# Optimization experiments

Hardware: AMD Instinct MI355X
Metric: run time of the kernel (lower is better)

The kernel has to match this reference:

```python
import jax, jax.numpy as jnp
import numpy as np

H = 200  # LSTM units per layer
SEQ_LEN = 100
NUM_AXIS = 4


def setup_inputs() -> dict:
    key = jax.random.key(0)
    ks = jax.random.split(key, 12)
    B = 8192
    s = 0.05  # small init scale to avoid gate saturation
    inp = {
        "x": jax.random.normal(ks[0], (B, SEQ_LEN, 1), dtype=jnp.float32),
        # layer 0: input dim 1
        "W0": jax.random.normal(ks[1], (1, 4 * H), dtype=jnp.float32) * s,
        "U0": jax.random.normal(ks[2], (H, 4 * H), dtype=jnp.float32) * s,
        "b0": jax.random.normal(ks[3], (4 * H,), dtype=jnp.float32) * s,
        # layer 1
        "W1": jax.random.normal(ks[4], (H, 4 * H), dtype=jnp.float32) * s,
        "U1": jax.random.normal(ks[5], (H, 4 * H), dtype=jnp.float32) * s,
        "b1": jax.random.normal(ks[6], (4 * H,), dtype=jnp.float32) * s,
        # layer 2
        "W2": jax.random.normal(ks[7], (H, 4 * H), dtype=jnp.float32) * s,
        "U2": jax.random.normal(ks[8], (H, 4 * H), dtype=jnp.float32) * s,
        "b2": jax.random.normal(ks[9], (4 * H,), dtype=jnp.float32) * s,
        # dense head: 200 -> 400, tanh
        "Wfc": jax.random.normal(ks[10], (H, SEQ_LEN * NUM_AXIS), dtype=jnp.float32) * s,
        "bfc": jax.random.normal(ks[11], (SEQ_LEN * NUM_AXIS,), dtype=jnp.float32) * s,
    }
    return inp


def _lstm_step(h, c, xt, W, U, b):
    # Keras LSTMCell gate order: i, f, g(candidate), o
    z = xt @ W + h @ U + b  # [B, 4H]
    i, f, g, o = jnp.split(z, 4, axis=-1)
    c_new = jax.nn.sigmoid(f) * c + jax.nn.sigmoid(i) * jnp.tanh(g)
    h_new = jax.nn.sigmoid(o) * jnp.tanh(c_new)
    return h_new, c_new


def reference(x, W0, U0, b0, W1, U1, b1, W2, U2, b2, Wfc, bfc):
    B = x.shape[0]
    zeros = jnp.zeros((B, H), dtype=x.dtype)
    carry0 = (zeros, zeros, zeros, zeros, zeros, zeros)

    def step(carry, xt):
        h0, c0, h1, c1, h2, c2 = carry
        h0, c0 = _lstm_step(h0, c0, xt, W0, U0, b0)
        h1, c1 = _lstm_step(h1, c1, h0, W1, U1, b1)
        h2, c2 = _lstm_step(h2, c2, h1, W2, U2, b2)
        return (h0, c0, h1, c1, h2, c2), None

    # scan over time: x is [B, T, 1] -> [T, B, 1]
    xs = jnp.swapaxes(x, 0, 1)
    (h0, c0, h1, c1, h2, c2), _ = jax.lax.scan(step, carry0, xs)
    # return_sequences=False -> final top-layer hidden state
    y = jnp.tanh(h2 @ Wfc + bfc)  # [B, 400]
    return y.reshape(B, SEQ_LEN, NUM_AXIS)
```

## Files before the change

kernel.cpp:

```cpp
#include <hip/hip_runtime.h>

#define Hdim 200
#define NP   800
#define Tlen 100
#define BT   32
#define KB   7
#define HS   232
#define NT   50
#define THREADS 768
#define CHSTR (NT*64*8)
#define MATSZ (KB*CHSTR)

#define WAIT_LGKM0 0xC07F

typedef float f32x4 __attribute__((ext_vector_type(4)));
typedef short s16x8 __attribute__((ext_vector_type(8)));

__device__ __forceinline__ ushort f2bf(float f) {
    unsigned u = __float_as_uint(f);
    return (ushort)((u + 0x7fffu + ((u >> 16) & 1u)) >> 16);
}
__device__ __forceinline__ float bf2f(ushort s) {
    return __uint_as_float(((unsigned)s) << 16);
}
__device__ __forceinline__ float sigmoid_fast(float v) {
    return 1.0f / (1.0f + __expf(-v));
}
__device__ __forceinline__ float tanh_fast(float v) {
    return 2.0f / (1.0f + __expf(-2.0f * v)) - 1.0f;
}
__device__ __forceinline__ void wg_barrier() {
    asm volatile("" ::: "memory");
    __builtin_amdgcn_s_waitcnt(WAIT_LGKM0);
    __builtin_amdgcn_s_barrier();
    asm volatile("" ::: "memory");
}

__global__ void pack_weights(const float* __restrict__ U0, const float* __restrict__ W1,
                             const float* __restrict__ U1, const float* __restrict__ W2,
                             const float* __restrict__ U2, ushort* __restrict__ dst) {
    int idx = blockIdx.x * blockDim.x + threadIdx.x;
    if (idx >= 5 * KB * NT * 64) return;
    int lane = idx & 63; int rest = idx >> 6;
    int nt = rest % NT; rest /= NT;
    int kb = rest % KB; int mi = rest / KB;
    const float* src = (mi == 0) ? U0 : (mi == 1) ? W1 : (mi == 2) ? U1 : (mi == 3) ? W2 : U2;
    int np = nt * 16 + (lane & 15);
    int ncol = (np & 3) * Hdim + (np >> 2);
    int k0 = kb * 32 + (lane >> 4) * 8;
    ushort v[8];
#pragma unroll
    for (int j = 0; j < 8; ++j) {
        int k = k0 + j;
        v[j] = (k < Hdim) ? f2bf(src[k * NP + ncol]) : (ushort)0;
    }
    uint4 o;
    o.x = (unsigned)v[0] | ((unsigned)v[1] << 16);
    o.y = (unsigned)v[2] | ((unsigned)v[3] << 16);
    o.z = (unsigned)v[4] | ((unsigned)v[5] << 16);
    o.w = (unsigned)v[6] | ((unsigned)v[7] << 16);
    ((uint4*)dst)[idx] = o;
}

template<int CHW>
__device__ __forceinline__ void stage_chunk(const ushort* gp, ushort* dstbuf, int lane) {
#pragma unroll
    for (int mt = 0; mt < CHW; ++mt) {
        __builtin_amdgcn_global_load_lds(
            (const __attribute__((address_space(1))) void*)(gp + (size_t)mt * 512 + lane * 8),
            (__attribute__((address_space(3))) void*)(dstbuf + mt * 512),
            16, 0, 0);
    }
}

__device__ __forceinline__ void unpack4(const ushort* p, float (&o)[4]) {
    uint2 u = *(const uint2*)p;
    o[0] = bf2f((ushort)(u.x));  o[1] = bf2f((ushort)(u.x >> 16));
    o[2] = bf2f((ushort)(u.y));  o[3] = bf2f((ushort)(u.y >> 16));
}

template<int CHW>
__device__ __forceinline__ void gate_phase(f32x4 (&acc)[2][CHW],
                                           float (&creg)[2][CHW],
                                           ushort* __restrict__ hbl,
                                           int lane, int S_w) {
    const int l15 = lane & 15, q = lane >> 4;
#pragma unroll
    for (int nt = 0; nt < 2; ++nt) {
#pragma unroll
        for (int mt = 0; mt < CHW; ++mt) {
            const int u = (S_w + mt) * 4 + q;
            const int n = nt * 16 + l15;
            f32x4 z = acc[nt][mt];
            float iv = sigmoid_fast(z[0]);
            float fv = sigmoid_fast(z[1]);
            float gv = tanh_fast(z[2]);
            float ov = sigmoid_fast(z[3]);
            float c = fv * creg[nt][mt] + iv * gv;
            creg[nt][mt] = c;
            hbl[n * HS + u] = f2bf(ov * tanh_fast(c));
        }
    }
}

template<int CHW>
__device__ __forceinline__ void run_slots(int s0, int s1, int t,
        ushort* __restrict__ sl, f32x4 (&acc)[2][CHW],
        const ushort* __restrict__ pk, const uint* gTab, const uint* bhTab,
        const ushort* hbflat, int bhbase, int lane, int& isl) {
#pragma unroll 1
    for (int s = s0; s < s1; ++s) {
        __builtin_amdgcn_s_waitcnt(0x0F70 | CHW);
        ushort* buf = sl + ((t + s) & 1) * (CHW * 512);
        s16x8 frag[CHW];
#pragma unroll
        for (int mt = 0; mt < CHW; ++mt)
            frag[mt] = *(const s16x8*)(buf + mt * 512 + lane * 8);
        const ushort* bp = hbflat + bhTab[s] + bhbase;
        s16x8 bh0 = *(const s16x8*)bp;
        s16x8 bh1 = *(const s16x8*)(bp + 16 * HS);
#pragma unroll
        for (int mt = 0; mt < CHW; ++mt) {
            acc[0][mt] = __builtin_amdgcn_mfma_f32_16x16x32_bf16(frag[mt], bh0, acc[0][mt], 0, 0, 0);
            acc[1][mt] = __builtin_amdgcn_mfma_f32_16x16x32_bf16(frag[mt], bh1, acc[1][mt], 0, 0, 0);
        }
        __builtin_amdgcn_s_waitcnt(WAIT_LGKM0);
        stage_chunk<CHW>(pk + gTab[isl], buf, lane);
        isl = (isl == 34) ? 0 : isl + 1;
    }
}

template<int CHW>
__device__ __forceinline__ void time_loop(const int S_w, const int lane,
        const int bhbase, ushort* __restrict__ sl, const ushort* __restrict__ pk,
        const uint* gTab, const uint* bhTab, ushort* __restrict__ hbflat,
        const ushort (&pbwb)[4][NP], const ushort (&xTs)[Tlen][BT]) {
    const int l15 = lane & 15, q = lane >> 4;

    float creg[3][2][CHW];
#pragma unroll
    for (int l = 0; l < 3; ++l)
#pragma unroll
        for (int nt = 0; nt < 2; ++nt)
#pragma unroll
            for (int mt = 0; mt < CHW; ++mt) creg[l][nt][mt] = 0.0f;

    stage_chunk<CHW>(pk + gTab[0], sl, lane);
    stage_chunk<CHW>(pk + gTab[1], sl + CHW * 512, lane);
    int isl = 2;

    for (int t = 0; t < Tlen; ++t) {
        f32x4 acc[2][CHW];

        const float xn0 = bf2f(xTs[t][l15]);
        const float xn1 = bf2f(xTs[t][16 + l15]);
#pragma unroll
        for (int mt = 0; mt < CHW; ++mt) {
            const int row = (S_w + mt) * 16 + q * 4;
            float bb[4], ww[4];
            unpack4(&pbwb[0][row], bb);
            unpack4(&pbwb[3][row], ww);
#pragma unroll
            for (int r = 0; r < 4; ++r) {
                acc[0][mt][r] = fmaf(xn0, ww[r], bb[r]);
                acc[1][mt][r] = fmaf(xn1, ww[r], bb[r]);
            }
        }

        run_slots<CHW>(0, 7, t, sl, acc, pk, gTab, bhTab, hbflat, bhbase, lane, isl);
        wg_barrier();
        gate_phase<CHW>(acc, creg[0], hbflat + 0 * BT * HS, lane, S_w);
        wg_barrier();

#pragma unroll
        for (int mt = 0; mt < CHW; ++mt) {
            const int row = (S_w + mt) * 16 + q * 4;
            float bb[4];
            unpack4(&pbwb[1][row], bb);
#pragma unroll
            for (int r = 0; r < 4; ++r) { acc[0][mt][r] = bb[r]; acc[1][mt][r] = bb[r]; }
        }
        run_slots<CHW>(7, 21, t, sl, acc, pk, gTab, bhTab, hbflat, bhbase, lane, isl);
        wg_barrier();
        gate_phase<CHW>(acc, creg[1], hbflat + 1 * BT * HS, lane, S_w);
        wg_barrier();

#pragma unroll
        for (int mt = 0; mt < CHW; ++mt) {
            const int row = (S_w + mt) * 16 + q * 4;
            float bb[4];
            unpack4(&pbwb[2][row], bb);
#pragma unroll
            for (int r = 0; r < 4; ++r) { acc[0][mt][r] = bb[r]; acc[1][mt][r] = bb[r]; }
        }
        run_slots<CHW>(21, 35, t, sl, acc, pk, gTab, bhTab, hbflat, bhbase, lane, isl);
        wg_barrier();
        gate_phase<CHW>(acc, creg[2], hbflat + 2 * BT * HS, lane, S_w);
        wg_barrier();
    }
}

__global__ void __launch_bounds__(THREADS)
lstm3_mfma(const float* __restrict__ x,
           const float* __restrict__ W0, const float* __restrict__ b0,
           const float* __restrict__ b1, const float* __restrict__ b2,
           const float* __restrict__ Wfc, const float* __restrict__ bfc,
           const ushort* __restrict__ packed,
           float* __restrict__ out) {
    __shared__ ushort hb[3][BT][HS];
    __shared__ ushort stage[NT * 1024];
    __shared__ ushort pbwb[4][NP];
    __shared__ ushort xTs[Tlen][BT];
    __shared__ uint   gTab[35];
    __shared__ uint   bhTab[35];

    const int tid = threadIdx.x;
    const int wave = tid >> 6, lane = tid & 63;
    const int bx = blockIdx.x;
    const int bbase = bx * BT;

    for (int i = tid; i < 3 * BT * HS; i += THREADS) ((ushort*)hb)[i] = 0;
    for (int i = tid; i < NP; i += THREADS) {
        int nc = (i & 3) * Hdim + (i >> 2);
        pbwb[0][i] = f2bf(b0[nc]); pbwb[1][i] = f2bf(b1[nc]);
        pbwb[2][i] = f2bf(b2[nc]); pbwb[3][i] = f2bf(W0[nc]);
    }
    for (int i = tid; i < BT * Tlen; i += THREADS) {
        int m = i / Tlen, tt = i % Tlen;
        xTs[tt][m] = f2bf(x[(size_t)(bbase + m) * Tlen + tt]);
    }
    if (tid < 35) {
        int s = tid; uint goff, bhoff;
        if (s < 7) {
            int c = (s + bx) % 7;
            goff = 0u * MATSZ + c * CHSTR;           bhoff = 0u * BT * HS + c * 32;
        } else if (s < 21) {
            int c = (s - 7 + bx) % 14;
            if (c < 7) { goff = 2u * MATSZ + c * CHSTR;       bhoff = 1u * BT * HS + c * 32; }
            else       { goff = 1u * MATSZ + (c - 7) * CHSTR; bhoff = 0u * BT * HS + (c - 7) * 32; }
        } else {
            int c = (s - 21 + bx * 5) % 14;
            if (c < 7) { goff = 4u * MATSZ + c * CHSTR;       bhoff = 2u * BT * HS + c * 32; }
            else       { goff = 3u * MATSZ + (c - 7) * CHSTR; bhoff = 1u * BT * HS + (c - 7) * 32; }
        }
        gTab[s] = goff; bhTab[s] = bhoff;
    }
    __syncthreads();

    const int S_w = (wave < 2) ? wave * 5 : 10 + (wave - 2) * 4;
    const ushort* pk = packed + (size_t)S_w * 512;
    ushort* sl = &stage[S_w * 1024];
    ushort* hbflat = &hb[0][0][0];
    const int bhbase = (lane & 15) * HS + (lane >> 4) * 8;

    if (wave < 2) time_loop<5>(S_w, lane, bhbase, sl, pk, gTab, bhTab, hbflat, pbwb, xTs);
    else          time_loop<4>(S_w, lane, bhbase, sl, pk, gTab, bhTab, hbflat, pbwb, xTs);

    __syncthreads();

    for (int gidx = tid; gidx < BT * 100; gidx += THREADS) {
        int m = gidx / 100;
        int j4 = (gidx % 100) * 4;
        const ushort* h2 = &hb[2][m][0];
        float4 a4 = *(const float4*)(bfc + j4);
        float s0 = a4.x, s1 = a4.y, s2 = a4.z, s3 = a4.w;
        for (int k = 0; k < Hdim; ++k) {
            float hk = bf2f(h2[k]);
            float4 w4 = *(const float4*)(Wfc + (size_t)k * 400 + j4);
            s0 = fmaf(hk, w4.x, s0);
            s1 = fmaf(hk, w4.y, s1);
            s2 = fmaf(hk, w4.z, s2);
            s3 = fmaf(hk, w4.w, s3);
        }
        float4 o4;
        o4.x = tanh_fast(s0); o4.y = tanh_fast(s1);
        o4.z = tanh_fast(s2); o4.w = tanh_fast(s3);
        *(float4*)(out + (size_t)(bbase + m) * 400 + j4) = o4;
    }
}

extern "C" void kernel_launch(void* const* d_in, const int* in_sizes, int n_in,
                              void* d_out, int out_size, void* d_ws, size_t ws_size,
                              hipStream_t stream) {
    const float* x   = (const float*)d_in[0];
    const float* W0  = (const float*)d_in[1];
    const float* U0  = (const float*)d_in[2];
    const float* b0  = (const float*)d_in[3];
    const float* W1  = (const float*)d_in[4];
    const float* U1  = (const float*)d_in[5];
    const float* b1  = (const float*)d_in[6];
    const float* W2  = (const float*)d_in[7];
    const float* U2  = (const float*)d_in[8];
    const float* b2  = (const float*)d_in[9];
    const float* Wfc = (const float*)d_in[10];
    const float* bfc = (const float*)d_in[11];
    float* out = (float*)d_out;
    ushort* packed = (ushort*)d_ws;

    const int B = in_sizes[0] / Tlen;
    const int pack_threads = 5 * KB * NT * 64;
    pack_weights<<<(pack_threads + 255) / 256, 256, 0, stream>>>(U0, W1, U1, W2, U2, packed);
    lstm3_mfma<<<B / BT, THREADS, 0, stream>>>(x, W0, b0, b1, b2, Wfc, bfc, packed, out);
}
```

Before: 2.644 ms.

## Keep two layer-0 weight chunks register-resident and stage Wfc through LDS for head

Each wave now loads its first two layer-0 recurrent weight chunks into registers once and computes those slots without DMA staging. This shrinks the per-step streamed ring from 35 to 33 slots and cuts global weight traffic and staging waits. The dense head is restructured to copy Wfc in 50-row chunks into the freed shared stage buffer, so the batch rows reuse it instead of each thread streaming Wfc from global memory. The cost is higher register pressure from the resident fragments, which could lower occupancy or cause spills.

```diff
diff --git a/kernel.cpp b/kernel.cpp
--- a/kernel.cpp
+++ b/kernel.cpp
@@ -10,6 +10,7 @@
 #define THREADS 768
 #define CHSTR (NT*64*8)
 #define MATSZ (KB*CHSTR)
+#define NRING 33
 
 #define WAIT_LGKM0 0xC07F
 
@@ -103,15 +104,28 @@
     }
 }
 
+template<int CHW, int C>
+__device__ __forceinline__ void res_slot(const s16x8 (&rw)[CHW], f32x4 (&acc)[2][CHW],
+        const ushort* hbflat, int bhbase) {
+    const ushort* bp = hbflat + C * 32 + bhbase;
+    s16x8 bh0 = *(const s16x8*)bp;
+    s16x8 bh1 = *(const s16x8*)(bp + 16 * HS);
+#pragma unroll
+    for (int mt = 0; mt < CHW; ++mt) {
+        acc[0][mt] = __builtin_amdgcn_mfma_f32_16x16x32_bf16(rw[mt], bh0, acc[0][mt], 0, 0, 0);
+        acc[1][mt] = __builtin_amdgcn_mfma_f32_16x16x32_bf16(rw[mt], bh1, acc[1][mt], 0, 0, 0);
+    }
+}
+
 template<int CHW>
-__device__ __forceinline__ void run_slots(int s0, int s1, int t,
+__device__ __forceinline__ void run_dma(int s0, int s1,
         ushort* __restrict__ sl, f32x4 (&acc)[2][CHW],
         const ushort* __restrict__ pk, const uint* gTab, const uint* bhTab,
-        const ushort* hbflat, int bhbase, int lane, int& isl) {
+        const ushort* hbflat, int bhbase, int lane, int& isl, int& par) {
 #pragma unroll 1
     for (int s = s0; s < s1; ++s) {
         __builtin_amdgcn_s_waitcnt(0x0F70 | CHW);
-        ushort* buf = sl + ((t + s) & 1) * (CHW * 512);
+        ushort* buf = sl + par * (CHW * 512);
         s16x8 frag[CHW];
 #pragma unroll
         for (int mt = 0; mt < CHW; ++mt)
@@ -126,7 +140,8 @@
         }
         __builtin_amdgcn_s_waitcnt(WAIT_LGKM0);
         stage_chunk<CHW>(pk + gTab[isl], buf, lane);
-        isl = (isl == 34) ? 0 : isl + 1;
+        isl = (isl == NRING - 1) ? 0 : isl + 1;
+        par ^= 1;
     }
 }
 
@@ -145,9 +160,16 @@
 #pragma unroll
             for (int mt = 0; mt < CHW; ++mt) creg[l][nt][mt] = 0.0f;
 
+    s16x8 rw0[CHW], rw1[CHW];
+#pragma unroll
+    for (int mt = 0; mt < CHW; ++mt) {
+        rw0[mt] = *(const s16x8*)(pk + 0 * CHSTR + mt * 512 + lane * 8);
+        rw1[mt] = *(const s16x8*)(pk + 1 * CHSTR + mt * 512 + lane * 8);
+    }
+
     stage_chunk<CHW>(pk + gTab[0], sl, lane);
     stage_chunk<CHW>(pk + gTab[1], sl + CHW * 512, lane);
-    int isl = 2;
+    int isl = 2, par = 0;
 
     for (int t = 0; t < Tlen; ++t) {
         f32x4 acc[2][CHW];
@@ -167,7 +189,11 @@
             }
         }
 
-        run_slots<CHW>(0, 7, t, sl, acc, pk, gTab, bhTab, hbflat, bhbase, lane, isl);
+        run_dma<CHW>(0, 1, sl, acc, pk, gTab, bhTab, hbflat, bhbase, lane, isl, par);
+        res_slot<CHW, 0>(rw0, acc, hbflat, bhbase);
+        run_dma<CHW>(1, 2, sl, acc, pk, gTab, bhTab, hbflat, bhbase, lane, isl, par);
+        res_slot<CHW, 1>(rw1, acc, hbflat, bhbase);
+        run_dma<CHW>(2, 5, sl, acc, pk, gTab, bhTab, hbflat, bhbase, lane, isl, par);
         wg_barrier();
         gate_phase<CHW>(acc, creg[0], hbflat + 0 * BT * HS, lane, S_w);
         wg_barrier();
@@ -180,7 +206,7 @@
 #pragma unroll
             for (int r = 0; r < 4; ++r) { acc[0][mt][r] = bb[r]; acc[1][mt][r] = bb[r]; }
         }
-        run_slots<CHW>(7, 21, t, sl, acc, pk, gTab, bhTab, hbflat, bhbase, lane, isl);
+        run_dma<CHW>(5, 19, sl, acc, pk, gTab, bhTab, hbflat, bhbase, lane, isl, par);
         wg_barrier();
         gate_phase<CHW>(acc, creg[1], hbflat + 1 * BT * HS, lane, S_w);
         wg_barrier();
@@ -193,7 +219,7 @@
 #pragma unroll
             for (int r = 0; r < 4; ++r) { acc[0][mt][r] = bb[r]; acc[1][mt][r] = bb[r]; }
         }
-        run_slots<CHW>(21, 35, t, sl, acc, pk, gTab, bhTab, hbflat, bhbase, lane, isl);
+        run_dma<CHW>(19, 33, sl, acc, pk, gTab, bhTab, hbflat, bhbase, lane, isl, par);
         wg_barrier();
         gate_phase<CHW>(acc, creg[2], hbflat + 2 * BT * HS, lane, S_w);
         wg_barrier();
@@ -211,8 +237,8 @@
     __shared__ ushort stage[NT * 1024];
     __shared__ ushort pbwb[4][NP];
     __shared__ ushort xTs[Tlen][BT];
-    __shared__ uint   gTab[35];
-    __shared__ uint   bhTab[35];
+    __shared__ uint   gTab[NRING];
+    __shared__ uint   bhTab[NRING];
 
     const int tid = threadIdx.x;
     const int wave = tid >> 6, lane = tid & 63;
@@ -229,21 +255,21 @@
         int m = i / Tlen, tt = i % Tlen;
         xTs[tt][m] = f2bf(x[(size_t)(bbase + m) * Tlen + tt]);
     }
-    if (tid < 35) {
-        int s = tid; uint goff, bhoff;
-        if (s < 7) {
-            int c = (s + bx) % 7;
+    if (tid < NRING) {
+        int r = tid; uint goff, bhoff;
+        if (r < 5) {
+            int c = 2 + (r + bx) % 5;
             goff = 0u * MATSZ + c * CHSTR;           bhoff = 0u * BT * HS + c * 32;
-        } else if (s < 21) {
-            int c = (s - 7 + bx) % 14;
+        } else if (r < 19) {
+            int c = (r - 5 + bx) % 14;
             if (c < 7) { goff = 2u * MATSZ + c * CHSTR;       bhoff = 1u * BT * HS + c * 32; }
             else       { goff = 1u * MATSZ + (c - 7) * CHSTR; bhoff = 0u * BT * HS + (c - 7) * 32; }
         } else {
-            int c = (s - 21 + bx * 5) % 14;
+            int c = (r - 19 + bx * 5) % 14;
             if (c < 7) { goff = 4u * MATSZ + c * CHSTR;       bhoff = 2u * BT * HS + c * 32; }
             else       { goff = 3u * MATSZ + (c - 7) * CHSTR; bhoff = 1u * BT * HS + (c - 7) * 32; }
         }
-        gTab[s] = goff; bhTab[s] = bhoff;
+        gTab[r] = goff; bhTab[r] = bhoff;
     }
     __syncthreads();
 
@@ -258,24 +284,47 @@
 
     __syncthreads();
 
-    for (int gidx = tid; gidx < BT * 100; gidx += THREADS) {
-        int m = gidx / 100;
-        int j4 = (gidx % 100) * 4;
-        const ushort* h2 = &hb[2][m][0];
-        float4 a4 = *(const float4*)(bfc + j4);
-        float s0 = a4.x, s1 = a4.y, s2 = a4.z, s3 = a4.w;
-        for (int k = 0; k < Hdim; ++k) {
-            float hk = bf2f(h2[k]);
-            float4 w4 = *(const float4*)(Wfc + (size_t)k * 400 + j4);
-            s0 = fmaf(hk, w4.x, s0);
-            s1 = fmaf(hk, w4.y, s1);
-            s2 = fmaf(hk, w4.z, s2);
-            s3 = fmaf(hk, w4.w, s3);
-        }
-        float4 o4;
-        o4.x = tanh_fast(s0); o4.y = tanh_fast(s1);
-        o4.z = tanh_fast(s2); o4.w = tanh_fast(s3);
-        *(float4*)(out + (size_t)(bbase + m) * 400 + j4) = o4;
+    float* wbuf = (float*)stage;
+    float4 a4[5];
+#pragma unroll
+    for (int r = 0; r < 5; ++r) {
+        int gidx = tid + r * THREADS;
+        if (gidx < BT * 100) a4[r] = *(const float4*)(bfc + (gidx % 100) * 4);
+    }
+    for (int kc = 0; kc < 4; ++kc) {
+        __syncthreads();
+        for (int i = tid; i < 50 * 400; i += THREADS)
+            wbuf[i] = Wfc[kc * 50 * 400 + i];
+        __syncthreads();
+#pragma unroll
+        for (int r = 0; r < 5; ++r) {
+            int gidx = tid + r * THREADS;
+            if (gidx < BT * 100) {
+                int m = gidx / 100, j4 = (gidx % 100) * 4;
+                const ushort* h2 = &hb[2][m][kc * 50];
+                float4 s = a4[r];
+                for (int k = 0; k < 50; ++k) {
+                    float hk = bf2f(h2[k]);
+                    float4 w4 = *(const float4*)(wbuf + k * 400 + j4);
+                    s.x = fmaf(hk, w4.x, s.x);
+                    s.y = fmaf(hk, w4.y, s.y);
+                    s.z = fmaf(hk, w4.z, s.z);
+                    s.w = fmaf(hk, w4.w, s.w);
+                }
+                a4[r] = s;
+            }
+        }
+    }
+#pragma unroll
+    for (int r = 0; r < 5; ++r) {
+        int gidx = tid + r * THREADS;
+        if (gidx < BT * 100) {
+            int m = gidx / 100, j4 = (gidx % 100) * 4;
+            float4 o4;
+            o4.x = tanh_fast(a4[r].x); o4.y = tanh_fast(a4[r].y);
+            o4.z = tanh_fast(a4[r].z); o4.w = tanh_fast(a4[r].w);
+            *(float4*)(out + (size_t)(bbase + m) * 400 + j4) = o4;
+        }
     }
 }
 
```

Result: slower. 3.392 ms (+28.3%).
